# Performance work log

Measured on AMD Instinct MI355X. Metric: run time of the kernel, lower is better.

Reference implementation:

```python
import jax, jax.numpy as jnp
import numpy as np

B, N = 4, 512
H, NH, L = 64, 4, 3
HD = H // NH          # 16
NODE_F, EDGE_F = 18, 7
H4 = H // 4           # 16
FF = 4 * H            # 256


def _ln(x, g, b, eps=1e-5):
    m = jnp.mean(x, axis=-1, keepdims=True)
    v = jnp.mean((x - m) ** 2, axis=-1, keepdims=True)
    return (x - m) * jax.lax.rsqrt(v + eps) * g + b


def _leaky(x):
    return jnp.where(x >= 0, x, 0.2 * x)


def _spd(edge_mask):
    # Vectorized Floyd-Warshall, mirrors GraphTransformer._compute_spd_matrix
    n = edge_mask.shape[1]
    spd = jnp.where(edge_mask, 1.0, float(n)).astype(jnp.float32)
    i = jnp.arange(n)
    spd = spd.at[:, i, i].set(0.0)
    def body(k, s):
        col = jax.lax.dynamic_slice_in_dim(s, k, 1, axis=2)  # [B,N,1]
        row = jax.lax.dynamic_slice_in_dim(s, k, 1, axis=1)  # [B,1,N]
        return jnp.minimum(s, col + row)
    return jax.lax.fori_loop(0, n, body, spd)


def setup_inputs() -> dict:
    key = jax.random.key(0)
    ks = iter(jax.random.split(key, 64))
    def nrm(shape, s):
        return jax.random.normal(next(ks), shape, jnp.float32) * s
    inp = {}
    inp["node_features"] = jax.random.normal(next(ks), (B, N, NODE_F), jnp.float32)
    inp["edge_features"] = jax.random.normal(next(ks), (B, N, N, EDGE_F), jnp.float32)
    nm = jax.random.uniform(next(ks), (B, N)) < 0.9
    inp["node_mask"] = nm.at[:, 0].set(True)
    inp["edge_mask"] = jax.random.uniform(next(ks), (B, N, N)) < 0.05
    s_h = 1.0 / np.sqrt(H)
    inp["node_proj_w"] = nrm((NODE_F, H), 0.2)
    inp["node_proj_b"] = jnp.zeros((H,), jnp.float32)
    inp["edge_proj_w"] = nrm((EDGE_F, H), 0.2)
    inp["edge_proj_b"] = jnp.zeros((H,), jnp.float32)
    inp["wq"] = nrm((L, H, H), s_h)
    inp["wk"] = nrm((L, H, H), s_h)
    inp["wv"] = nrm((L, H, H), s_h)
    inp["eb1_w"] = nrm((L, H, H4), s_h)
    inp["eb1_b"] = jnp.zeros((L, H4), jnp.float32)
    inp["eb_ln_g"] = jnp.ones((L, H4), jnp.float32)
    inp["eb_ln_b"] = jnp.zeros((L, H4), jnp.float32)
    inp["eb2_w"] = nrm((L, H4, NH), 0.2)
    inp["eb2_b"] = jnp.zeros((L, NH), jnp.float32)
    inp["spd1_w"] = nrm((L, 1, H4), 0.5)
    inp["spd1_b"] = jnp.zeros((L, H4), jnp.float32)
    inp["spd2_w"] = nrm((L, H4, NH), 0.2)
    inp["spd2_b"] = jnp.zeros((L, NH), jnp.float32)
    inp["wo_w"] = nrm((L, H, H), s_h)
    inp["wo_b"] = jnp.zeros((L, H), jnp.float32)
    inp["ln1_g"] = jnp.ones((L, H), jnp.float32)
    inp["ln1_b"] = jnp.zeros((L, H), jnp.float32)
    inp["ln2_g"] = jnp.ones((L, H), jnp.float32)
    inp["ln2_b"] = jnp.zeros((L, H), jnp.float32)
    inp["ffn1_w"] = nrm((L, H, FF), s_h)
    inp["ffn1_b"] = jnp.zeros((L, FF), jnp.float32)
    inp["ffn2_w"] = nrm((L, FF, H), 1.0 / np.sqrt(FF))
    inp["ffn2_b"] = jnp.zeros((L, H), jnp.float32)
    inp["score1_w"] = nrm((2 * H, H), 1.0 / np.sqrt(2 * H))
    inp["score1_b"] = jnp.zeros((H,), jnp.float32)
    inp["score_ln_g"] = jnp.ones((H,), jnp.float32)
    inp["score_ln_b"] = jnp.zeros((H,), jnp.float32)
    inp["score2_w"] = nrm((H, 1), 0.1)
    inp["score2_b"] = jnp.zeros((1,), jnp.float32)
    return inp


def reference(node_features, edge_features, node_mask, edge_mask,
              node_proj_w, node_proj_b, edge_proj_w, edge_proj_b,
              wq, wk, wv,
              eb1_w, eb1_b, eb_ln_g, eb_ln_b, eb2_w, eb2_b,
              spd1_w, spd1_b, spd2_w, spd2_b,
              wo_w, wo_b, ln1_g, ln1_b, ln2_g, ln2_b,
              ffn1_w, ffn1_b, ffn2_w, ffn2_b,
              score1_w, score1_b, score_ln_g, score_ln_b, score2_w, score2_b):
    NEG = -1000000000.0
    h = node_features @ node_proj_w + node_proj_b            # [B,N,H]
    e = edge_features @ edge_proj_w + edge_proj_b            # [B,N,N,H]
    spd = _spd(edge_mask)
    spd_n = (jnp.clip(spd, 0.0, 10.0) / 10.0)[..., None]      # [B,N,N,1]
    scale = 1.0 / np.sqrt(HD)
    for l in range(L):
        Q = (h @ wq[l]).reshape(B, N, NH, HD)
        K = (h @ wk[l]).reshape(B, N, NH, HD)
        V = (h @ wv[l]).reshape(B, N, NH, HD)
        scores = jnp.einsum('bihd,bjhd->bhij', Q, K) * scale  # [B,NH,N,N]
        x = _leaky(_ln(e @ eb1_w[l] + eb1_b[l], eb_ln_g[l], eb_ln_b[l]))
        edge_bias = jnp.transpose(x @ eb2_w[l] + eb2_b[l], (0, 3, 1, 2))
        sb = _leaky(spd_n @ spd1_w[l] + spd1_b[l]) @ spd2_w[l] + spd2_b[l]
        spd_bias = jnp.transpose(sb, (0, 3, 1, 2))
        bias = jnp.where(edge_mask[:, None, :, :], edge_bias, spd_bias)
        scores = jnp.where(node_mask[:, None, None, :], scores + bias, NEG)
        attn = jax.nn.softmax(scores, axis=-1)
        out = jnp.einsum('bhij,bjhd->bihd', attn, V).reshape(B, N, H)
        out = out @ wo_w[l] + wo_b[l]
        h = _ln(h + out, ln1_g[l], ln1_b[l])
        ff = jax.nn.gelu(h @ ffn1_w[l] + ffn1_b[l], approximate=False) @ ffn2_w[l] + ffn2_b[l]
        h = _ln(h + ff, ln2_g[l], ln2_b[l])
    h_ego = jnp.broadcast_to(h[:, :1, :], (B, N - 1, H))
    hc = jnp.concatenate([h_ego, h[:, 1:, :]], axis=-1)       # [B,N-1,2H]
    x = _leaky(_ln(hc @ score1_w + score1_b, score_ln_g, score_ln_b))
    logits = (x @ score2_w + score2_b)[..., 0]                # [B,N-1]
    cand_mask = node_mask[:, 1:]
    no_cand = ~jnp.any(cand_mask, axis=-1)
    cand_mask = cand_mask.at[:, 0].set(cand_mask[:, 0] | no_cand)
    logits = jnp.where(cand_mask, logits, NEG)
    probs = jax.nn.softmax(logits, axis=-1)
    return probs, h
```

## Files before the change

### kernel.cpp

```cpp
#include <hip/hip_runtime.h>
#include <math.h>

typedef unsigned long long u64;
typedef unsigned int u32;

__device__ __forceinline__ float wsum(float x) {
#pragma unroll
    for (int o = 1; o < 64; o <<= 1) x += __shfl_xor(x, o);
    return x;
}
__device__ __forceinline__ float wmaxr(float x) {
#pragma unroll
    for (int o = 1; o < 64; o <<= 1) x = fmaxf(x, __shfl_xor(x, o));
    return x;
}

__global__ __launch_bounds__(256) void kA(
    const int* __restrict__ em, const float* __restrict__ nf,
    const float* __restrict__ npw, const float* __restrict__ npb,
    u64* __restrict__ adj, u32* __restrict__ elist, u32* __restrict__ rowCnt,
    float* __restrict__ hbuf)
{
    int t = threadIdx.x, wv = t >> 6, lane = t & 63;
    int g = blockIdx.x * 4 + wv;
    const int* emr = em + (size_t)g * 512;
    u32 run = 0;
#pragma unroll
    for (int s = 0; s < 8; ++s) {
        int j = s * 64 + lane;
        int v = emr[j];
        u64 bal = __ballot(v != 0);
        if (v != 0) {
            u32 slot = run + (u32)__popcll(bal & ((1ULL << lane) - 1ULL));
            if (slot < 96u) elist[g * 96 + slot] = (u32)j;
        }
        if (lane == 0) adj[(size_t)g * 8 + s] = bal;
        run += (u32)__popcll(bal);
    }
    if (lane == 0) rowCnt[g] = run < 96u ? run : 96u;
    float acc = npb[lane];
    const float* r = nf + (size_t)g * 18;
#pragma unroll
    for (int c = 0; c < 18; ++c) acc += r[c] * npw[c * 64 + lane];
    hbuf[(size_t)g * 64 + lane] = acc;
}

__global__ __launch_bounds__(256) void kB(
    const u64* __restrict__ adj, const float* __restrict__ ef,
    const u32* __restrict__ elist, const u32* __restrict__ rowCnt,
    const float* __restrict__ hbuf,
    const float* __restrict__ epw, const float* __restrict__ epb,
    const float* __restrict__ eb1w, const float* __restrict__ eb1b,
    const float* __restrict__ eblng, const float* __restrict__ eblnb,
    const float* __restrict__ eb2w, const float* __restrict__ eb2b,
    const float* __restrict__ wq, const float* __restrict__ wk, const float* __restrict__ wvw,
    unsigned char* __restrict__ spd, float* __restrict__ vals,
    float* __restrict__ Qb, float* __restrict__ KT, float* __restrict__ VT)
{
    __shared__ u64 adjL[4096];
    __shared__ u64 bfsS[4][24];
    __shared__ float MS[684];
    __shared__ u32 pool[384];
    __shared__ u32 offs[5];
    __shared__ u32 cA[4];
    __shared__ int votes[4];
    int t = threadIdx.x, wv = t >> 6, lane = t & 63;
    int g = blockIdx.x * 4 + wv;
    int b = g >> 9, srow = g & 511;
    {
        const float4* s = (const float4*)(adj + (size_t)b * 4096);
        float4* d = (float4*)adjL;
#pragma unroll
        for (int u = 0; u < 8; ++u) d[t + u * 256] = s[t + u * 256];
    }
    for (int u = t; u < 384; u += 256) {
        int l = u >> 7, r = u & 127, f = r >> 4, c = r & 15;
        const float* W1 = eb1w + l * 1024 + c;
        float s;
        if (f < 7) {
            s = 0.f;
            const float* ew = epw + f * 64;
            for (int k = 0; k < 64; ++k) s += ew[k] * W1[k * 16];
        } else {
            s = eb1b[l * 16 + c];
            for (int k = 0; k < 64; ++k) s += epb[k] * W1[k * 16];
        }
        MS[u] = s;
    }
    if (t < 192) MS[384 + t] = eb2w[t];
    if (t < 48) { MS[576 + t] = eblng[t]; MS[624 + t] = eblnb[t]; }
    if (t < 12) MS[672 + t] = eb2b[t];
    u64* vis = &bfsS[wv][0]; u64* fro = vis + 8; u64* nxt = vis + 16;
    if (lane < 8) {
        u64 iv = (lane == (srow >> 6)) ? (1ULL << (srow & 63)) : 0ULL;
        vis[lane] = iv; fro[lane] = iv; nxt[lane] = 0ULL;
    }
    __syncthreads();
    u64 myDist = 0x0A0A0A0A0A0A0A0AULL;
    if (lane == (srow >> 3)) myDist &= ~(0xFFULL << ((srow & 7) * 8));
    for (int d = 1; d <= 9; ++d) {
        int c = lane >> 3, w = lane & 7;
        u64 f = fro[c];
        u64 acc = 0ULL;
        while (f) {
            int k = (c << 6) + __builtin_ctzll(f);
            f &= f - 1;
            acc |= adjL[k * 8 + w];
        }
        if (acc) atomicOr(&nxt[w], acc);
        __syncthreads();
        u64 nw = 0ULL;
        if (lane < 8) {
            nw = nxt[lane] & ~vis[lane];
            vis[lane] |= nw; fro[lane] = nw; nxt[lane] = 0ULL;
        }
        u64 bal = __ballot(nw != 0ULL);
        if (lane == 0) votes[wv] = (bal != 0ULL) ? 1 : 0;
        __syncthreads();
        u64 fw = fro[lane >> 3];
        u32 bits = (u32)(fw >> ((lane & 7) * 8)) & 0xFFu;
        if (bits) {
            u64 bm = 0ULL;
#pragma unroll
            for (int kk = 0; kk < 8; ++kk) if (bits & (1u << kk)) bm |= 0xFFULL << (8 * kk);
            myDist = (myDist & ~bm) | ((0x0101010101010101ULL * (u64)(u32)d) & bm);
        }
        if (!(votes[0] | votes[1] | votes[2] | votes[3])) break;
    }
    ((u64*)spd)[(size_t)g * 64 + lane] = myDist;
    {
        float hv = hbuf[(size_t)g * 64 + lane];
        float aq = 0.f, ak = 0.f, av = 0.f;
        for (int k = 0; k < 64; ++k) {
            float hk = __shfl(hv, k);
            aq += hk * wq[k * 64 + lane];
            ak += hk * wk[k * 64 + lane];
            av += hk * wvw[k * 64 + lane];
        }
        Qb[(size_t)g * 64 + lane] = aq;
        KT[((size_t)(b * 64 + lane)) * 512 + srow] = ak;
        VT[((size_t)(b * 64 + lane)) * 512 + srow] = av;
    }
    u32 cnt = rowCnt[g];
    if (lane == 0) cA[wv] = cnt;
    __syncthreads();
    if (t == 0) {
        u32 a = 0;
        for (int i = 0; i < 4; ++i) { offs[i] = a; a += cA[i]; }
        offs[4] = a;
    }
    __syncthreads();
    u32 base = offs[wv];
    if (lane < (int)cnt)
        pool[base + lane] = ((u32)wv << 16) | ((u32)lane << 9) | elist[g * 96 + lane];
    if (lane + 64 < (int)cnt)
        pool[base + lane + 64] = ((u32)wv << 16) | ((u32)(lane + 64) << 9) | elist[g * 96 + lane + 64];
    __syncthreads();
    u32 tot = offs[4];
    for (u32 e = t; e < tot; e += 256) {
        u32 p = pool[e];
        int rl = (int)(p >> 16);
        u32 s = (p >> 9) & 127u;
        u32 j = p & 511u;
        int ge = blockIdx.x * 4 + rl;
        const float* e7 = ef + ((size_t)ge * 512 + j) * 7;
        float ff[7];
#pragma unroll
        for (int f = 0; f < 7; ++f) ff[f] = e7[f];
#pragma unroll 1
        for (int l = 0; l < 3; ++l) {
            float tt[16];
#pragma unroll
            for (int c = 0; c < 16; ++c) tt[c] = MS[(l * 8 + 7) * 16 + c];
#pragma unroll
            for (int f = 0; f < 7; ++f) {
                float fv = ff[f];
#pragma unroll
                for (int c = 0; c < 16; ++c) tt[c] += fv * MS[(l * 8 + f) * 16 + c];
            }
            float m = 0.f;
#pragma unroll
            for (int c = 0; c < 16; ++c) m += tt[c];
            m *= 0.0625f;
            float var = 0.f;
#pragma unroll
            for (int c = 0; c < 16; ++c) { float d = tt[c] - m; var += d * d; }
            var *= 0.0625f;
            float inv = rsqrtf(var + 1e-5f);
#pragma unroll
            for (int c = 0; c < 16; ++c) {
                float x = (tt[c] - m) * inv * MS[576 + l * 16 + c] + MS[624 + l * 16 + c];
                tt[c] = x >= 0.f ? x : 0.2f * x;
            }
#pragma unroll
            for (int hh = 0; hh < 4; ++hh) {
                float a = MS[672 + l * 4 + hh];
#pragma unroll
                for (int c = 0; c < 16; ++c) a += tt[c] * MS[384 + (l * 16 + c) * 4 + hh];
                vals[(u32)(l * 4 + hh) * 196608u + (u32)ge * 96u + s] = a;
            }
        }
    }
}

__global__ __launch_bounds__(256, 2) void kAttn(
    const float* __restrict__ Qb, const float* __restrict__ KTin, const float* __restrict__ VTin,
    const unsigned char* __restrict__ spd, const u32* __restrict__ elist,
    const u32* __restrict__ rowCnt, const float* __restrict__ vals,
    const float* __restrict__ s1w, const float* __restrict__ s1b,
    const float* __restrict__ s2w, const float* __restrict__ s2b,
    const int* __restrict__ nm, int l, float* __restrict__ attO)
{
    __shared__ float kt[8192];
    __shared__ float bv[8192];
    int t = threadIdx.x, wv = t >> 6, lane = t & 63;
    int bh = blockIdx.x >> 5;
    int tile = blockIdx.x & 31;
    int b = bh >> 2, hh = bh & 3;
    int i0 = tile * 16;
    int rbase = i0 + wv * 4;
    float qv = Qb[((size_t)(b * 512 + rbase + (lane >> 4))) * 64 + hh * 16 + (lane & 15)];
    float q[4][16];
#pragma unroll
    for (int r = 0; r < 4; ++r)
#pragma unroll
        for (int d = 0; d < 16; ++d) q[r][d] = __shfl(qv, r * 16 + d);
    {
        const float4* s = (const float4*)(KTin + ((size_t)(b * 64 + hh * 16)) * 512);
        float4* d = (float4*)kt;
#pragma unroll
        for (int u = 0; u < 8; ++u) d[t + u * 256] = s[t + u * 256];
    }
    float tval;
    {
        int li = lane < 11 ? lane : 10;
        float x = (float)li * 0.1f;
        float a = s2b[l * 4 + hh];
#pragma unroll
        for (int c = 0; c < 16; ++c) {
            float v = x * s1w[l * 16 + c] + s1b[l * 16 + c];
            v = v >= 0.f ? v : 0.2f * v;
            a += v * s2w[(l * 16 + c) * 4 + hh];
        }
        tval = a;
    }
    {
        const u32* sp = (const u32*)(spd + ((size_t)(b * 512 + i0)) * 512);
#pragma unroll
        for (int p = 0; p < 8; ++p) {
            int i32 = t + p * 256;
            u32 w4 = sp[i32];
            float4 bb;
            bb.x = __shfl(tval, (int)(w4 & 255u));
            bb.y = __shfl(tval, (int)((w4 >> 8) & 255u));
            bb.z = __shfl(tval, (int)((w4 >> 16) & 255u));
            bb.w = __shfl(tval, (int)(w4 >> 24));
            ((float4*)bv)[i32] = bb;
        }
    }
    __syncthreads();
    u32 vp = (u32)(l * 4 + hh) * 196608u;
#pragma unroll
    for (int rr = 0; rr < 4; ++rr) {
        int g = b * 512 + rbase + rr;
        u32 cnt = rowCnt[g];
        for (u32 s = lane; s < cnt; s += 64u) {
            u32 j = elist[g * 96 + s] & 511u;
            bv[(wv * 4 + rr) * 512 + j] = vals[vp + (u32)g * 96u + s];
        }
    }
    const int* nmb = nm + b * 512;
    float sc[8][4];
    float mx[4] = {-3e38f, -3e38f, -3e38f, -3e38f};
#pragma unroll
    for (int c = 0; c < 8; ++c) {
        int j = c * 64 + lane;
        float ktv[16];
#pragma unroll
        for (int d = 0; d < 16; ++d) ktv[d] = kt[d * 512 + j];
        float madd = (nmb[j] != 0) ? 0.f : -1e9f;
#pragma unroll
        for (int r = 0; r < 4; ++r) {
            float s = 0.f;
#pragma unroll
            for (int d = 0; d < 16; ++d) s += q[r][d] * ktv[d];
            s = s * 0.25f + bv[(wv * 4 + r) * 512 + j] + madd;
            sc[c][r] = s;
            mx[r] = fmaxf(mx[r], s);
        }
    }
#pragma unroll
    for (int r = 0; r < 4; ++r) mx[r] = wmaxr(mx[r]);
    float sm[4] = {0.f, 0.f, 0.f, 0.f};
#pragma unroll
    for (int c = 0; c < 8; ++c)
#pragma unroll
        for (int r = 0; r < 4; ++r) { sc[c][r] = __expf(sc[c][r] - mx[r]); sm[r] += sc[c][r]; }
#pragma unroll
    for (int r = 0; r < 4; ++r) sm[r] = 1.0f / wsum(sm[r]);
#pragma unroll
    for (int c = 0; c < 8; ++c)
#pragma unroll
        for (int r = 0; r < 4; ++r) sc[c][r] *= sm[r];
    __syncthreads();
    {
        const float4* s = (const float4*)(VTin + ((size_t)(b * 64 + hh * 16)) * 512);
        float4* d = (float4*)kt;
#pragma unroll
        for (int u = 0; u < 8; ++u) d[t + u * 256] = s[t + u * 256];
    }
    __syncthreads();
    float acc[4][16];
#pragma unroll
    for (int r = 0; r < 4; ++r)
#pragma unroll
        for (int d = 0; d < 16; ++d) acc[r][d] = 0.f;
#pragma unroll
    for (int c = 0; c < 8; ++c) {
        int j = c * 64 + lane;
#pragma unroll
        for (int d = 0; d < 16; ++d) {
            float v = kt[d * 512 + j];
#pragma unroll
            for (int r = 0; r < 4; ++r) acc[r][d] += sc[c][r] * v;
        }
    }
#pragma unroll
    for (int r = 0; r < 4; ++r)
#pragma unroll
        for (int d = 0; d < 16; ++d) {
            acc[r][d] += __shfl_xor(acc[r][d], 16);
            acc[r][d] += __shfl_xor(acc[r][d], 32);
        }
    float* scr = bv + wv * 2048;
    if (lane < 16) {
#pragma unroll
        for (int r = 0; r < 4; ++r)
#pragma unroll
            for (int d = 0; d < 16; ++d) scr[lane * 65 + r * 16 + d] = acc[r][d];
    }
    float o = 0.f;
#pragma unroll
    for (int m = 0; m < 16; ++m) o += scr[m * 65 + lane];
    attO[((size_t)(b * 512 + rbase + (lane >> 4))) * 64 + hh * 16 + (lane & 15)] = o;
}

__global__ __launch_bounds__(256) void kLF(
    const float* __restrict__ attO,
    const float* __restrict__ wow, const float* __restrict__ wob,
    const float* __restrict__ ln1g, const float* __restrict__ ln1b,
    const float* __restrict__ f1w, const float* __restrict__ f1b,
    const float* __restrict__ f2w, const float* __restrict__ f2b,
    const float* __restrict__ ln2g, const float* __restrict__ ln2b,
    const float* __restrict__ wqn, const float* __restrict__ wkn, const float* __restrict__ wvn,
    const float* __restrict__ sc1w, const float* __restrict__ sc1b,
    float* __restrict__ hbuf, float* __restrict__ QbOut,
    float* __restrict__ KTout, float* __restrict__ VTout,
    float* __restrict__ egoAcc, int l, float* __restrict__ out)
{
    int t = threadIdx.x, wv = t >> 6, lane = t & 63;
    int g = blockIdx.x * 4 + wv;
    int b = g >> 9, srow = g & 511;
    float hv = hbuf[(size_t)g * 64 + lane];
    float att = attO[(size_t)g * 64 + lane];
    float h1;
    {
        float a = wob[l * 64 + lane];
        const float* Wo = wow + l * 4096;
        for (int k = 0; k < 64; ++k) a += __shfl(att, k) * Wo[k * 64 + lane];
        float xx = a + hv;
        float mn = wsum(xx) * 0.015625f;
        float d = xx - mn;
        float var = wsum(d * d) * 0.015625f;
        h1 = d * rsqrtf(var + 1e-5f) * ln1g[l * 64 + lane] + ln1b[l * 64 + lane];
    }
    float hn;
    {
        const float* W1 = f1w + l * 16384;
        const float* W2 = f2w + l * 16384;
        float a1[4];
#pragma unroll
        for (int m = 0; m < 4; ++m) a1[m] = f1b[l * 256 + m * 64 + lane];
        for (int k = 0; k < 64; ++k) {
            float hk = __shfl(h1, k);
#pragma unroll
            for (int m = 0; m < 4; ++m) a1[m] += hk * W1[k * 256 + m * 64 + lane];
        }
        float ffv[4];
#pragma unroll
        for (int m = 0; m < 4; ++m) {
            float u = a1[m];
            ffv[m] = 0.5f * u * (1.0f + erff(u * 0.70710678118654752f));
        }
        float a2p0 = 0.f, a2p1 = 0.f, a2p2 = 0.f, a2p3 = 0.f;
        for (int ll = 0; ll < 64; ++ll) {
            a2p0 += __shfl(ffv[0], ll) * W2[(ll) * 64 + lane];
            a2p1 += __shfl(ffv[1], ll) * W2[(64 + ll) * 64 + lane];
            a2p2 += __shfl(ffv[2], ll) * W2[(128 + ll) * 64 + lane];
            a2p3 += __shfl(ffv[3], ll) * W2[(192 + ll) * 64 + lane];
        }
        float a2 = ((a2p0 + a2p1) + a2p2) + a2p3;
        float xx = a2 + f2b[l * 64 + lane] + h1;
        float mn = wsum(xx) * 0.015625f;
        float d = xx - mn;
        float var = wsum(d * d) * 0.015625f;
        hn = d * rsqrtf(var + 1e-5f) * ln2g[l * 64 + lane] + ln2b[l * 64 + lane];
    }
    hbuf[(size_t)g * 64 + lane] = hn;
    if (l == 2) {
        out[2044 + (size_t)g * 64 + lane] = hn;
        if (srow == 0) {
            float ea = sc1b[lane];
            for (int k = 0; k < 64; ++k) ea += __shfl(hn, k) * sc1w[k * 64 + lane];
            egoAcc[b * 64 + lane] = ea;
        }
    } else {
        float aq = 0.f, ak = 0.f, av = 0.f;
        for (int k = 0; k < 64; ++k) {
            float hk = __shfl(hn, k);
            aq += hk * wqn[k * 64 + lane];
            ak += hk * wkn[k * 64 + lane];
            av += hk * wvn[k * 64 + lane];
        }
        QbOut[(size_t)g * 64 + lane] = aq;
        KTout[((size_t)(b * 64 + lane)) * 512 + srow] = ak;
        VTout[((size_t)(b * 64 + lane)) * 512 + srow] = av;
    }
}

__global__ __launch_bounds__(256) void kS(
    const float* __restrict__ hbuf, const float* __restrict__ egoAcc,
    const float* __restrict__ s1w,
    const float* __restrict__ lng, const float* __restrict__ lnb,
    const float* __restrict__ s2w, const float* __restrict__ s2b,
    float* __restrict__ logits)
{
    int t = threadIdx.x, wv = t >> 6, lane = t & 63;
    int wid = blockIdx.x * 4 + wv;
    if (wid >= 2044) return;
    int bb = wid / 511; int jj = wid % 511; int j = jj + 1;
    float cand = hbuf[((size_t)(bb * 512 + j)) * 64 + lane];
    float acc = egoAcc[bb * 64 + lane];
    for (int k = 0; k < 64; ++k) acc += __shfl(cand, k) * s1w[(64 + k) * 64 + lane];
    float mn = wsum(acc) * 0.015625f;
    float d = acc - mn;
    float var = wsum(d * d) * 0.015625f;
    float x = d * rsqrtf(var + 1e-5f) * lng[lane] + lnb[lane];
    x = x >= 0.f ? x : 0.2f * x;
    float p = wsum(x * s2w[lane]);
    if (lane == 0) logits[wid] = p + s2b[0];
}

__global__ __launch_bounds__(512) void kP(
    const float* __restrict__ logits, const int* __restrict__ nmask, float* __restrict__ out)
{
    __shared__ float red[512];
    __shared__ int anyf;
    int b = blockIdx.x; int t = threadIdx.x;
    bool cand = false;
    if (t < 511) cand = nmask[b * 512 + 1 + t] != 0;
    if (t == 0) anyf = 0;
    __syncthreads();
    if (cand) atomicOr(&anyf, 1);
    __syncthreads();
    if (t == 0 && anyf == 0) cand = true;
    float val = -3e38f;
    if (t < 511) val = cand ? logits[b * 511 + t] : -1e9f;
    red[t] = val; __syncthreads();
    for (int s = 256; s > 0; s >>= 1) { if (t < s) red[t] = fmaxf(red[t], red[t + s]); __syncthreads(); }
    float m = red[0]; __syncthreads();
    float p = (t < 511) ? __expf(val - m) : 0.f;
    red[t] = p; __syncthreads();
    for (int s = 256; s > 0; s >>= 1) { if (t < s) red[t] += red[t + s]; __syncthreads(); }
    float inv = 1.0f / red[0];
    if (t < 511) out[b * 511 + t] = p * inv;
}

extern "C" void kernel_launch(void* const* d_in, const int* in_sizes, int n_in,
                              void* d_out, int out_size, void* d_ws, size_t ws_size,
                              hipStream_t stream) {
    const float* nf    = (const float*)d_in[0];
    const float* ef    = (const float*)d_in[1];
    const int*   nm    = (const int*)d_in[2];
    const int*   em    = (const int*)d_in[3];
    const float* npw   = (const float*)d_in[4];
    const float* npb   = (const float*)d_in[5];
    const float* epw   = (const float*)d_in[6];
    const float* epb   = (const float*)d_in[7];
    const float* wq    = (const float*)d_in[8];
    const float* wk    = (const float*)d_in[9];
    const float* wv    = (const float*)d_in[10];
    const float* eb1w  = (const float*)d_in[11];
    const float* eb1b  = (const float*)d_in[12];
    const float* eblng = (const float*)d_in[13];
    const float* eblnb = (const float*)d_in[14];
    const float* eb2w  = (const float*)d_in[15];
    const float* eb2b  = (const float*)d_in[16];
    const float* s1wv  = (const float*)d_in[17];
    const float* s1bv  = (const float*)d_in[18];
    const float* s2wv  = (const float*)d_in[19];
    const float* s2bv  = (const float*)d_in[20];
    const float* wow   = (const float*)d_in[21];
    const float* wob   = (const float*)d_in[22];
    const float* ln1g  = (const float*)d_in[23];
    const float* ln1b  = (const float*)d_in[24];
    const float* ln2g  = (const float*)d_in[25];
    const float* ln2b  = (const float*)d_in[26];
    const float* f1w   = (const float*)d_in[27];
    const float* f1b   = (const float*)d_in[28];
    const float* f2w   = (const float*)d_in[29];
    const float* f2b   = (const float*)d_in[30];
    const float* sc1w  = (const float*)d_in[31];
    const float* sc1b  = (const float*)d_in[32];
    const float* sclng = (const float*)d_in[33];
    const float* sclnb = (const float*)d_in[34];
    const float* sc2w  = (const float*)d_in[35];
    const float* sc2b  = (const float*)d_in[36];

    char* W = (char*)d_ws;
    u64*   adj    = (u64*)(W + 0);
    unsigned char* spd = (unsigned char*)(W + 131072);
    u32*   elist  = (u32*)(W + 1179648);
    u32*   rowCnt = (u32*)(W + 1966080);
    float* vals   = (float*)(W + 1974272);
    float* hbuf   = (float*)(W + 11411456);
    float* Qb     = (float*)(W + 11935744);
    float* KT0    = (float*)(W + 12460032);
    float* VT0    = (float*)(W + 12984320);
    float* KT1    = (float*)(W + 13508608);
    float* VT1    = (float*)(W + 14032896);
    float* logits = (float*)(W + 14557184);
    float* egoAcc = (float*)(W + 14565376);
    float* attO   = (float*)(W + 14566400);

    float* out = (float*)d_out;

    kA<<<512, 256, 0, stream>>>(em, nf, npw, npb, adj, elist, rowCnt, hbuf);
    kB<<<512, 256, 0, stream>>>(adj, ef, elist, rowCnt, hbuf, epw, epb,
                                eb1w, eb1b, eblng, eblnb, eb2w, eb2b,
                                wq, wk, wv, spd, vals, Qb, KT0, VT0);

    kAttn<<<512, 256, 0, stream>>>(Qb, KT0, VT0, spd, elist, rowCnt, vals,
                                   s1wv, s1bv, s2wv, s2bv, nm, 0, attO);
    kLF<<<512, 256, 0, stream>>>(attO, wow, wob, ln1g, ln1b, f1w, f1b, f2w, f2b,
                                 ln2g, ln2b, wq + 4096, wk + 4096, wv + 4096,
                                 sc1w, sc1b, hbuf, Qb, KT1, VT1, egoAcc, 0, out);

    kAttn<<<512, 256, 0, stream>>>(Qb, KT1, VT1, spd, elist, rowCnt, vals,
                                   s1wv, s1bv, s2wv, s2bv, nm, 1, attO);
    kLF<<<512, 256, 0, stream>>>(attO, wow, wob, ln1g, ln1b, f1w, f1b, f2w, f2b,
                                 ln2g, ln2b, wq + 8192, wk + 8192, wv + 8192,
                                 sc1w, sc1b, hbuf, Qb, KT0, VT0, egoAcc, 1, out);

    kAttn<<<512, 256, 0, stream>>>(Qb, KT0, VT0, spd, elist, rowCnt, vals,
                                   s1wv, s1bv, s2wv, s2bv, nm, 2, attO);
    kLF<<<512, 256, 0, stream>>>(attO, wow, wob, ln1g, ln1b, f1w, f1b, f2w, f2b,
                                 ln2g, ln2b, wq, wk, wv,
                                 sc1w, sc1b, hbuf, Qb, KT1, VT1, egoAcc, 2, out);

    kS<<<511, 256, 0, stream>>>(hbuf, egoAcc, sc1w, sclng, sclnb, sc2w, sc2b, logits);
    kP<<<4, 512, 0, stream>>>(logits, nm, out);
}
```

Baseline: 284.3 us.

## Fuse attention and FFN layer kernels via last-arriving-block counters

Merges the per-layer attention kernel and the output-projection/FFN/LayerNorm/QKV kernel into one. Each block bumps an atomic counter for its (batch, row-tile) after storing its head's attention output. The fourth block to arrive for that tile then runs the dense tail for those 16 rows. The counters are zeroed in the first kernel. This removes one launch and the global barrier per layer, at the cost of running the dense tail on only a quarter of the blocks, with each wave handling four rows in sequence, which may lengthen the kernel's tail.

```diff
diff --git a/kernel.cpp b/kernel.cpp
--- a/kernel.cpp
+++ b/kernel.cpp
@@ -13,16 +13,26 @@
 #pragma unroll
     for (int o = 1; o < 64; o <<= 1) x = fmaxf(x, __shfl_xor(x, o));
     return x;
+}
+__device__ __forceinline__ float cldf(const float* p) {
+    return __hip_atomic_load(p, __ATOMIC_RELAXED, __HIP_MEMORY_SCOPE_AGENT);
+}
+__device__ __forceinline__ void cstf(float* p, float v) {
+    __hip_atomic_store(p, v, __ATOMIC_RELAXED, __HIP_MEMORY_SCOPE_AGENT);
 }
 
 __global__ __launch_bounds__(256) void kA(
     const int* __restrict__ em, const float* __restrict__ nf,
     const float* __restrict__ npw, const float* __restrict__ npb,
     u64* __restrict__ adj, u32* __restrict__ elist, u32* __restrict__ rowCnt,
-    float* __restrict__ hbuf)
+    float* __restrict__ hbuf, u32* __restrict__ tcnt)
 {
     int t = threadIdx.x, wv = t >> 6, lane = t & 63;
     int g = blockIdx.x * 4 + wv;
+    if (blockIdx.x == 0) {
+        for (int u = t; u < 384; u += 256)
+            __hip_atomic_store(&tcnt[u], 0u, __ATOMIC_RELAXED, __HIP_MEMORY_SCOPE_AGENT);
+    }
     const int* emr = em + (size_t)g * 512;
     u32 run = 0;
 #pragma unroll
@@ -203,16 +213,28 @@
     }
 }
 
-__global__ __launch_bounds__(256, 2) void kAttn(
+__global__ __launch_bounds__(256, 2) void kAttnF(
     const float* __restrict__ Qb, const float* __restrict__ KTin, const float* __restrict__ VTin,
     const unsigned char* __restrict__ spd, const u32* __restrict__ elist,
     const u32* __restrict__ rowCnt, const float* __restrict__ vals,
     const float* __restrict__ s1w, const float* __restrict__ s1b,
     const float* __restrict__ s2w, const float* __restrict__ s2b,
-    const int* __restrict__ nm, int l, float* __restrict__ attO)
+    const int* __restrict__ nm,
+    const float* __restrict__ wow, const float* __restrict__ wob,
+    const float* __restrict__ ln1g, const float* __restrict__ ln1b,
+    const float* __restrict__ f1w, const float* __restrict__ f1b,
+    const float* __restrict__ f2w, const float* __restrict__ f2b,
+    const float* __restrict__ ln2g, const float* __restrict__ ln2b,
+    const float* __restrict__ wqn, const float* __restrict__ wkn, const float* __restrict__ wvn,
+    const float* __restrict__ sc1w, const float* __restrict__ sc1b,
+    float* __restrict__ attO, float* __restrict__ hbuf,
+    float* __restrict__ KTout, float* __restrict__ VTout,
+    float* __restrict__ egoAcc, u32* __restrict__ tcnt,
+    int l, float* __restrict__ out)
 {
     __shared__ float kt[8192];
     __shared__ float bv[8192];
+    __shared__ int doneS;
     int t = threadIdx.x, wv = t >> 6, lane = t & 63;
     int bh = blockIdx.x >> 5;
     int tile = blockIdx.x & 31;
@@ -342,89 +364,84 @@
     float o = 0.f;
 #pragma unroll
     for (int m = 0; m < 16; ++m) o += scr[m * 65 + lane];
-    attO[((size_t)(b * 512 + rbase + (lane >> 4))) * 64 + hh * 16 + (lane & 15)] = o;
-}
-
-__global__ __launch_bounds__(256) void kLF(
-    const float* __restrict__ attO,
-    const float* __restrict__ wow, const float* __restrict__ wob,
-    const float* __restrict__ ln1g, const float* __restrict__ ln1b,
-    const float* __restrict__ f1w, const float* __restrict__ f1b,
-    const float* __restrict__ f2w, const float* __restrict__ f2b,
-    const float* __restrict__ ln2g, const float* __restrict__ ln2b,
-    const float* __restrict__ wqn, const float* __restrict__ wkn, const float* __restrict__ wvn,
-    const float* __restrict__ sc1w, const float* __restrict__ sc1b,
-    float* __restrict__ hbuf, float* __restrict__ QbOut,
-    float* __restrict__ KTout, float* __restrict__ VTout,
-    float* __restrict__ egoAcc, int l, float* __restrict__ out)
-{
-    int t = threadIdx.x, wv = t >> 6, lane = t & 63;
-    int g = blockIdx.x * 4 + wv;
-    int b = g >> 9, srow = g & 511;
-    float hv = hbuf[(size_t)g * 64 + lane];
-    float att = attO[(size_t)g * 64 + lane];
-    float h1;
-    {
-        float a = wob[l * 64 + lane];
-        const float* Wo = wow + l * 4096;
-        for (int k = 0; k < 64; ++k) a += __shfl(att, k) * Wo[k * 64 + lane];
-        float xx = a + hv;
-        float mn = wsum(xx) * 0.015625f;
-        float d = xx - mn;
-        float var = wsum(d * d) * 0.015625f;
-        h1 = d * rsqrtf(var + 1e-5f) * ln1g[l * 64 + lane] + ln1b[l * 64 + lane];
-    }
-    float hn;
-    {
-        const float* W1 = f1w + l * 16384;
-        const float* W2 = f2w + l * 16384;
-        float a1[4];
-#pragma unroll
-        for (int m = 0; m < 4; ++m) a1[m] = f1b[l * 256 + m * 64 + lane];
-        for (int k = 0; k < 64; ++k) {
-            float hk = __shfl(h1, k);
-#pragma unroll
-            for (int m = 0; m < 4; ++m) a1[m] += hk * W1[k * 256 + m * 64 + lane];
-        }
-        float ffv[4];
-#pragma unroll
-        for (int m = 0; m < 4; ++m) {
-            float u = a1[m];
-            ffv[m] = 0.5f * u * (1.0f + erff(u * 0.70710678118654752f));
-        }
-        float a2p0 = 0.f, a2p1 = 0.f, a2p2 = 0.f, a2p3 = 0.f;
-        for (int ll = 0; ll < 64; ++ll) {
-            a2p0 += __shfl(ffv[0], ll) * W2[(ll) * 64 + lane];
-            a2p1 += __shfl(ffv[1], ll) * W2[(64 + ll) * 64 + lane];
-            a2p2 += __shfl(ffv[2], ll) * W2[(128 + ll) * 64 + lane];
-            a2p3 += __shfl(ffv[3], ll) * W2[(192 + ll) * 64 + lane];
-        }
-        float a2 = ((a2p0 + a2p1) + a2p2) + a2p3;
-        float xx = a2 + f2b[l * 64 + lane] + h1;
-        float mn = wsum(xx) * 0.015625f;
-        float d = xx - mn;
-        float var = wsum(d * d) * 0.015625f;
-        hn = d * rsqrtf(var + 1e-5f) * ln2g[l * 64 + lane] + ln2b[l * 64 + lane];
-    }
-    hbuf[(size_t)g * 64 + lane] = hn;
-    if (l == 2) {
-        out[2044 + (size_t)g * 64 + lane] = hn;
-        if (srow == 0) {
-            float ea = sc1b[lane];
-            for (int k = 0; k < 64; ++k) ea += __shfl(hn, k) * sc1w[k * 64 + lane];
-            egoAcc[b * 64 + lane] = ea;
-        }
-    } else {
-        float aq = 0.f, ak = 0.f, av = 0.f;
-        for (int k = 0; k < 64; ++k) {
-            float hk = __shfl(hn, k);
-            aq += hk * wqn[k * 64 + lane];
-            ak += hk * wkn[k * 64 + lane];
-            av += hk * wvn[k * 64 + lane];
-        }
-        QbOut[(size_t)g * 64 + lane] = aq;
-        KTout[((size_t)(b * 64 + lane)) * 512 + srow] = ak;
-        VTout[((size_t)(b * 64 + lane)) * 512 + srow] = av;
+    cstf(attO + ((size_t)(b * 512 + rbase + (lane >> 4))) * 64 + hh * 16 + (lane & 15), o);
+    __syncthreads();
+    if (t == 0) {
+        doneS = (int)__hip_atomic_fetch_add(&tcnt[b * 32 + tile], 1u,
+                                            __ATOMIC_ACQ_REL, __HIP_MEMORY_SCOPE_AGENT);
+    }
+    __syncthreads();
+    if (doneS != 3) return;
+
+#pragma unroll 1
+    for (int rr = 0; rr < 4; ++rr) {
+        int g = b * 512 + rbase + rr;
+        int srow = g & 511;
+        float hv = hbuf[(size_t)g * 64 + lane];
+        float att = cldf(attO + (size_t)g * 64 + lane);
+        float h1;
+        {
+            float a = wob[l * 64 + lane];
+            const float* Wo = wow + l * 4096;
+            for (int k = 0; k < 64; ++k) a += __shfl(att, k) * Wo[k * 64 + lane];
+            float xx = a + hv;
+            float mn = wsum(xx) * 0.015625f;
+            float d = xx - mn;
+            float var = wsum(d * d) * 0.015625f;
+            h1 = d * rsqrtf(var + 1e-5f) * ln1g[l * 64 + lane] + ln1b[l * 64 + lane];
+        }
+        float hn;
+        {
+            const float* W1 = f1w + l * 16384;
+            const float* W2 = f2w + l * 16384;
+            float a1[4];
+#pragma unroll
+            for (int m = 0; m < 4; ++m) a1[m] = f1b[l * 256 + m * 64 + lane];
+            for (int k = 0; k < 64; ++k) {
+                float hk = __shfl(h1, k);
+#pragma unroll
+                for (int m = 0; m < 4; ++m) a1[m] += hk * W1[k * 256 + m * 64 + lane];
+            }
+            float ffv[4];
+#pragma unroll
+            for (int m = 0; m < 4; ++m) {
+                float u = a1[m];
+                ffv[m] = 0.5f * u * (1.0f + erff(u * 0.70710678118654752f));
+            }
+            float a2p0 = 0.f, a2p1 = 0.f, a2p2 = 0.f, a2p3 = 0.f;
+            for (int ll = 0; ll < 64; ++ll) {
+                a2p0 += __shfl(ffv[0], ll) * W2[(ll) * 64 + lane];
+                a2p1 += __shfl(ffv[1], ll) * W2[(64 + ll) * 64 + lane];
+                a2p2 += __shfl(ffv[2], ll) * W2[(128 + ll) * 64 + lane];
+                a2p3 += __shfl(ffv[3], ll) * W2[(192 + ll) * 64 + lane];
+            }
+            float a2 = ((a2p0 + a2p1) + a2p2) + a2p3;
+            float xx = a2 + f2b[l * 64 + lane] + h1;
+            float mn = wsum(xx) * 0.015625f;
+            float d = xx - mn;
+            float var = wsum(d * d) * 0.015625f;
+            hn = d * rsqrtf(var + 1e-5f) * ln2g[l * 64 + lane] + ln2b[l * 64 + lane];
+        }
+        hbuf[(size_t)g * 64 + lane] = hn;
+        if (l == 2) {
+            out[2044 + (size_t)g * 64 + lane] = hn;
+            if (srow == 0) {
+                float ea = sc1b[lane];
+                for (int k = 0; k < 64; ++k) ea += __shfl(hn, k) * sc1w[k * 64 + lane];
+                egoAcc[b * 64 + lane] = ea;
+            }
+        } else {
+            float aq = 0.f, ak = 0.f, av = 0.f;
+            for (int k = 0; k < 64; ++k) {
+                float hk = __shfl(hn, k);
+                aq += hk * wqn[k * 64 + lane];
+                ak += hk * wkn[k * 64 + lane];
+                av += hk * wvn[k * 64 + lane];
+            }
+            ((float*)Qb)[(size_t)g * 64 + lane] = aq;
+            KTout[((size_t)(b * 64 + lane)) * 512 + srow] = ak;
+            VTout[((size_t)(b * 64 + lane)) * 512 + srow] = av;
+        }
     }
 }
 
@@ -532,31 +549,30 @@
     float* logits = (float*)(W + 14557184);
     float* egoAcc = (float*)(W + 14565376);
     float* attO   = (float*)(W + 14566400);
+    u32*   tcnt   = (u32*)(W + 15090688);
 
     float* out = (float*)d_out;
 
-    kA<<<512, 256, 0, stream>>>(em, nf, npw, npb, adj, elist, rowCnt, hbuf);
+    kA<<<512, 256, 0, stream>>>(em, nf, npw, npb, adj, elist, rowCnt, hbuf, tcnt);
     kB<<<512, 256, 0, stream>>>(adj, ef, elist, rowCnt, hbuf, epw, epb,
                                 eb1w, eb1b, eblng, eblnb, eb2w, eb2b,
                                 wq, wk, wv, spd, vals, Qb, KT0, VT0);
 
-    kAttn<<<512, 256, 0, stream>>>(Qb, KT0, VT0, spd, elist, rowCnt, vals,
-                                   s1wv, s1bv, s2wv, s2bv, nm, 0, attO);
-    kLF<<<512, 256, 0, stream>>>(attO, wow, wob, ln1g, ln1b, f1w, f1b, f2w, f2b,
-                                 ln2g, ln2b, wq + 4096, wk + 4096, wv + 4096,
-                                 sc1w, sc1b, hbuf, Qb, KT1, VT1, egoAcc, 0, out);
-
-    kAttn<<<512, 256, 0, stream>>>(Qb, KT1, VT1, spd, elist, rowCnt, vals,
-                                   s1wv, s1bv, s2wv, s2bv, nm, 1, attO);
-    kLF<<<512, 256, 0, stream>>>(attO, wow, wob, ln1g, ln1b, f1w, f1b, f2w, f2b,
-                                 ln2g, ln2b, wq + 8192, wk + 8192, wv + 8192,
-                                 sc1w, sc1b, hbuf, Qb, KT0, VT0, egoAcc, 1, out);
-
-    kAttn<<<512, 256, 0, stream>>>(Qb, KT0, VT0, spd, elist, rowCnt, vals,
-                                   s1wv, s1bv, s2wv, s2bv, nm, 2, attO);
-    kLF<<<512, 256, 0, stream>>>(attO, wow, wob, ln1g, ln1b, f1w, f1b, f2w, f2b,
-                                 ln2g, ln2b, wq, wk, wv,
-                                 sc1w, sc1b, hbuf, Qb, KT1, VT1, egoAcc, 2, out);
+    kAttnF<<<512, 256, 0, stream>>>(Qb, KT0, VT0, spd, elist, rowCnt, vals,
+                                    s1wv, s1bv, s2wv, s2bv, nm,
+                                    wow, wob, ln1g, ln1b, f1w, f1b, f2w, f2b, ln2g, ln2b,
+                                    wq + 4096, wk + 4096, wv + 4096, sc1w, sc1b,
+                                    attO, hbuf, KT1, VT1, egoAcc, tcnt, 0, out);
+    kAttnF<<<512, 256, 0, stream>>>(Qb, KT1, VT1, spd, elist, rowCnt, vals,
+                                    s1wv, s1bv, s2wv, s2bv, nm,
+                                    wow, wob, ln1g, ln1b, f1w, f1b, f2w, f2b, ln2g, ln2b,
+                                    wq + 8192, wk + 8192, wv + 8192, sc1w, sc1b,
+                                    attO, hbuf, KT0, VT0, egoAcc, tcnt + 128, 1, out);
+    kAttnF<<<512, 256, 0, stream>>>(Qb, KT0, VT0, spd, elist, rowCnt, vals,
+                                    s1wv, s1bv, s2wv, s2bv, nm,
+                                    wow, wob, ln1g, ln1b, f1w, f1b, f2w, f2b, ln2g, ln2b,
+                                    wq, wk, wv, sc1w, sc1b,
+                                    attO, hbuf, KT1, VT1, egoAcc, tcnt + 256, 2, out);
 
     kS<<<511, 256, 0, stream>>>(hbuf, egoAcc, sc1w, sclng, sclnb, sc2w, sc2b, logits);
     kP<<<4, 512, 0, stream>>>(logits, nm, out);
```

New measurement: 418.0 us. 47.0% more time.
